# Optimization experiments

Hardware: AMD Instinct MI355X
Metric: run time of the kernel (lower is better)

Reference implementation:

```python
import jax, jax.numpy as jnp
import numpy as np

B, S, K, N = 2, 4096, 4096, 4096
BLOCKSIZE = 128  # GPTQ group size


def _unpack_rows(q):
    # int32 [K//8, N] -> int32 [K, N], 8 nibbles packed along dim 0 (little-endian)
    shifts = (jnp.arange(8, dtype=jnp.int32) * 4)
    nib = (q[:, None, :] >> shifts[None, :, None]) & 0xF  # [K//8, 8, N]
    return nib.reshape(q.shape[0] * 8, q.shape[1])


def _unpack_cols(q):
    # int32 [G, N//8] -> int32 [G, N], 8 nibbles packed along dim 1
    shifts = (jnp.arange(8, dtype=jnp.int32) * 4)
    nib = (q[:, :, None] >> shifts[None, None, :]) & 0xF  # [G, N//8, 8]
    return nib.reshape(q.shape[0], q.shape[1] * 8)


def _dequant(qweight, scales, qzeros, blocksize):
    # GPTQ int4 dequant: w[k, n] = (q[k, n] - z[g, n]) * s[g, n], g = k // blocksize
    w_int = _unpack_rows(qweight).astype(jnp.float32)          # [K, N]
    zeros = _unpack_cols(qzeros).astype(jnp.float32)           # [G, N]
    z = jnp.repeat(zeros, blocksize, axis=0)                   # [K, N]
    s = jnp.repeat(scales, blocksize, axis=0)                  # [K, N]
    return (w_int - z) * s


def setup_inputs() -> dict:
    key = jax.random.key(0)
    ks = jax.random.split(key, 6)
    inp = jax.random.normal(ks[0], (B, S, K), dtype=jnp.float32)
    residual = jax.random.normal(ks[1], (B, S, N), dtype=jnp.float32)
    qweight = jax.random.randint(ks[2], (K // 8, N), 0, 2147483647, dtype=jnp.int32)
    qzeros = jax.random.randint(ks[3], (K // BLOCKSIZE, N // 8), 0, 2147483647, dtype=jnp.int32)
    scales = jax.random.uniform(ks[4], (K // BLOCKSIZE, N), dtype=jnp.float32, minval=1e-3, maxval=1e-2)
    bias = jax.random.normal(ks[5], (N,), dtype=jnp.float32)
    return {"input": inp, "residual": residual, "qweight": qweight,
            "scales": scales, "qzeros": qzeros, "bias": bias}


def reference(input, residual, qweight, scales, qzeros, bias):
    # Fused: dequant(int4 GPTQ) -> GEMM -> +bias -> +residual (mm_bias_add_int4)
    w = _dequant(qweight, scales, qzeros, BLOCKSIZE)           # [K, N]
    out = jnp.einsum('bsk,kn->bsn', input, w) + bias + residual
    return out
```

## Files before the change

### kernel.cpp

```cpp
#include <hip/hip_runtime.h>
#include <hip/hip_bf16.h>
#include <stdint.h>

using bf16 = __hip_bfloat16;
typedef __attribute__((ext_vector_type(8))) short short8;
typedef __attribute__((ext_vector_type(4))) float floatx4;

#define DEVINL __device__ __forceinline__

constexpr int K_DIM = 4096;
constexpr int N_DIM = 4096;
constexpr int M_DIM = 8192;

constexpr int BM = 128, BN = 128, BK = 32;
constexpr int NBLK_N = N_DIM / BN;

DEVINL void gload_lds16(const void* g, void* l) {
  __builtin_amdgcn_global_load_lds((const __attribute__((address_space(1))) void*)g,
                                   (__attribute__((address_space(3))) void*)l,
                                   16, 0, 0);
}

__global__ __launch_bounds__(256) void k_a_convert(const float* __restrict__ a,
                                                   bf16* __restrict__ o) {
  int t = blockIdx.x * 256 + threadIdx.x;
  const float4* a4 = (const float4*)a;
  float4 v0 = a4[2 * t], v1 = a4[2 * t + 1];
  bf16 h[8];
  h[0] = __float2bfloat16(v0.x); h[1] = __float2bfloat16(v0.y);
  h[2] = __float2bfloat16(v0.z); h[3] = __float2bfloat16(v0.w);
  h[4] = __float2bfloat16(v1.x); h[5] = __float2bfloat16(v1.y);
  h[6] = __float2bfloat16(v1.z); h[7] = __float2bfloat16(v1.w);
  ((uint4*)o)[t] = *(const uint4*)h;
}

__global__ __launch_bounds__(256) void k_dequant(const int* __restrict__ qw,
                                                 const float* __restrict__ scales,
                                                 const int* __restrict__ qz,
                                                 bf16* __restrict__ wt) {
  __shared__ __align__(16) uint4 lds[32 * 8];
  const int b = blockIdx.x;
  const int kp0 = (b & 63) * 8;
  const int n0  = (b >> 6) * 32;
  const int t = threadIdx.x;
  const int n_l = t & 31, kp_l = t >> 5;
  const int n = n0 + n_l, kp = kp0 + kp_l;

  int q = qw[kp * N_DIM + n];
  int g = kp0 >> 4;
  float s = scales[g * N_DIM + n];
  int zword = qz[g * (N_DIM / 8) + (n >> 3)];
  float z = (float)((zword >> ((n & 7) * 4)) & 0xF);
  float nzs = -z * s;
  bf16 h[8];
#pragma unroll
  for (int i = 0; i < 8; ++i) {
    float w = fmaf((float)((q >> (4 * i)) & 0xF), s, nzs);
    h[i] = __float2bfloat16(w);
  }
  lds[n_l * 8 + (kp_l ^ (n_l & 7))] = *(const uint4*)h;
  __syncthreads();
  const int n_o = t >> 3, kp_o = t & 7;
  uint4 v = lds[n_o * 8 + (kp_o ^ (n_o & 7))];
  ((uint4*)wt)[(size_t)(n0 + n_o) * (K_DIM / 8) + kp0 + kp_o] = v;
}

template <bool A_IS_BF16>
__global__ __launch_bounds__(256, 2) void k_gemm(const void* __restrict__ a_ptr,
                                                 const bf16* __restrict__ wt,
                                                 const float* __restrict__ bias,
                                                 const float* __restrict__ residual,
                                                 float* __restrict__ out) {
  __shared__ __align__(16) bf16 As[BM * BK];
  __shared__ __align__(16) bf16 Bs[BN * BK];

  const int tid  = threadIdx.x;
  const int lane = tid & 63;
  const int wave = tid >> 6;
  const int wr = wave >> 1, wc = wave & 1;
  const int quad = lane >> 4, lq = lane & 15;
  const int sw = (lane >> 1) & 3;
  const int rd_c8 = (quad ^ sw) * 8;

  const int bid = blockIdx.x;
  const int bm = bid / NBLK_N, bn = bid % NBLK_N;
  const int m0 = bm * BM, n0 = bn * BN;

  floatx4 acc[4][4] = {};

  const int st_row = lane >> 2;
  const int st_c8  = ((lane & 3) ^ ((lane >> 3) & 3)) * 8;

  const bf16*  a_bf = (const bf16*)a_ptr;
  const float* a_f  = (const float*)a_ptr;

  for (int k0 = 0; k0 < K_DIM; k0 += BK) {
    __syncthreads();
#pragma unroll
    for (int j = 0; j < 2; ++j) {
      int q = wave + j * 4;
      const bf16* g = wt + (size_t)(n0 + q * 16 + st_row) * K_DIM + k0 + st_c8;
      gload_lds16(g, &Bs[q * 512]);
    }
    if (A_IS_BF16) {
#pragma unroll
      for (int j = 0; j < 2; ++j) {
        int q = wave + j * 4;
        const bf16* g = a_bf + (size_t)(m0 + q * 16 + st_row) * K_DIM + k0 + st_c8;
        gload_lds16(g, &As[q * 512]);
      }
    } else {
      int row = tid >> 1, c0 = (tid & 1) * 2;
      int rsw = (row >> 1) & 3;
      const float* srcf = a_f + (size_t)(m0 + row) * K_DIM + k0 + c0 * 8;
      float4 v0 = ((const float4*)srcf)[0];
      float4 v1 = ((const float4*)srcf)[1];
      float4 v2 = ((const float4*)srcf)[2];
      float4 v3 = ((const float4*)srcf)[3];
      bf16 h[16];
      h[0]  = __float2bfloat16(v0.x); h[1]  = __float2bfloat16(v0.y);
      h[2]  = __float2bfloat16(v0.z); h[3]  = __float2bfloat16(v0.w);
      h[4]  = __float2bfloat16(v1.x); h[5]  = __float2bfloat16(v1.y);
      h[6]  = __float2bfloat16(v1.z); h[7]  = __float2bfloat16(v1.w);
      h[8]  = __float2bfloat16(v2.x); h[9]  = __float2bfloat16(v2.y);
      h[10] = __float2bfloat16(v2.z); h[11] = __float2bfloat16(v2.w);
      h[12] = __float2bfloat16(v3.x); h[13] = __float2bfloat16(v3.y);
      h[14] = __float2bfloat16(v3.z); h[15] = __float2bfloat16(v3.w);
      *(uint4*)&As[row * BK + ((c0 ^ rsw) * 8)]       = *(const uint4*)h;
      *(uint4*)&As[row * BK + (((c0 + 1) ^ rsw) * 8)] = *(const uint4*)(h + 8);
    }
    __syncthreads();

    short8 afr[4], bfr[4];
#pragma unroll
    for (int mi = 0; mi < 4; ++mi)
      afr[mi] = *(const short8*)&As[(wr * 64 + mi * 16 + lq) * BK + rd_c8];
#pragma unroll
    for (int ni = 0; ni < 4; ++ni)
      bfr[ni] = *(const short8*)&Bs[(wc * 64 + ni * 16 + lq) * BK + rd_c8];
#pragma unroll
    for (int mi = 0; mi < 4; ++mi)
#pragma unroll
      for (int ni = 0; ni < 4; ++ni)
        acc[mi][ni] = __builtin_amdgcn_mfma_f32_16x16x32_bf16(afr[mi], bfr[ni],
                                                              acc[mi][ni], 0, 0, 0);
  }

#pragma unroll
  for (int ni = 0; ni < 4; ++ni) {
    int col = n0 + wc * 64 + ni * 16 + lq;
    float bv = bias[col];
#pragma unroll
    for (int mi = 0; mi < 4; ++mi) {
      int rbase = m0 + wr * 64 + mi * 16 + quad * 4;
#pragma unroll
      for (int r = 0; r < 4; ++r) {
        size_t idx = (size_t)(rbase + r) * N_DIM + col;
        out[idx] = acc[mi][ni][r] + bv + residual[idx];
      }
    }
  }
}

extern "C" void kernel_launch(void* const* d_in, const int* in_sizes, int n_in,
                              void* d_out, int out_size, void* d_ws, size_t ws_size,
                              hipStream_t stream) {
  const float* input    = (const float*)d_in[0];
  const float* residual = (const float*)d_in[1];
  const int*   qweight  = (const int*)d_in[2];
  const float* scales   = (const float*)d_in[3];
  const int*   qzeros   = (const int*)d_in[4];
  const float* bias     = (const float*)d_in[5];
  float* out = (float*)d_out;

  const size_t wt_bytes = (size_t)N_DIM * K_DIM * sizeof(bf16);
  const size_t a_bytes  = (size_t)M_DIM * K_DIM * sizeof(bf16);

  bf16* wt = (bf16*)d_ws;
  k_dequant<<<64 * 128, 256, 0, stream>>>(qweight, scales, qzeros, wt);

  if (ws_size >= wt_bytes + a_bytes) {
    bf16* a_bf = (bf16*)((char*)d_ws + wt_bytes);
    k_a_convert<<<(M_DIM * K_DIM / 8) / 256, 256, 0, stream>>>(input, a_bf);
    k_gemm<true><<<(M_DIM / BM) * (N_DIM / BN), 256, 0, stream>>>(a_bf, wt, bias, residual, out);
  } else {
    k_gemm<false><<<(M_DIM / BM) * (N_DIM / BN), 256, 0, stream>>>(input, wt, bias, residual, out);
  }
}
```

Baseline: 648.6 us.

## Double GEMM K-tile to 64 with 8-way XOR swizzle and XCD-aware block mapping

Raises the K tile from 32 to 64, so each loop iteration does two MFMA sub-steps and the number of barrier round trips halves. LDS loads and reads switch to an 8-chunk XOR swizzle to avoid bank conflicts on the wider rows. Blocks are remapped so that each XCD gets a contiguous group of 4 N-column tiles, which should improve L2 reuse of the weight tiles. The cost is more LDS per block (32KB instead of 16KB), which could limit occupancy.

```diff
diff --git a/kernel.cpp b/kernel.cpp
--- a/kernel.cpp
+++ b/kernel.cpp
@@ -12,8 +12,9 @@
 constexpr int N_DIM = 4096;
 constexpr int M_DIM = 8192;
 
-constexpr int BM = 128, BN = 128, BK = 32;
+constexpr int BM = 128, BN = 128, BK = 64;
 constexpr int NBLK_N = N_DIM / BN;
+constexpr int NBLK_M = M_DIM / BM;
 
 DEVINL void gload_lds16(const void* g, void* l) {
   __builtin_amdgcn_global_load_lds((const __attribute__((address_space(1))) void*)g,
@@ -79,17 +80,19 @@
   const int wave = tid >> 6;
   const int wr = wave >> 1, wc = wave & 1;
   const int quad = lane >> 4, lq = lane & 15;
-  const int sw = (lane >> 1) & 3;
-  const int rd_c8 = (quad ^ sw) * 8;
 
-  const int bid = blockIdx.x;
-  const int bm = bid / NBLK_N, bn = bid % NBLK_N;
+  const int xcd = blockIdx.x & 7;
+  const int idx = blockIdx.x >> 3;
+  const int bn = xcd * 4 + (idx & 3);
+  const int bm = idx >> 2;
   const int m0 = bm * BM, n0 = bn * BN;
 
   floatx4 acc[4][4] = {};
 
-  const int st_row = lane >> 2;
-  const int st_c8  = ((lane & 3) ^ ((lane >> 3) & 3)) * 8;
+  const int st_r8 = lane >> 3;
+  const int st_ce = ((lane & 7) ^ (st_r8 & 7)) * 8;
+
+  const int rd_x = lq & 7;
 
   const bf16*  a_bf = (const bf16*)a_ptr;
   const float* a_f  = (const float*)a_ptr;
@@ -97,53 +100,55 @@
   for (int k0 = 0; k0 < K_DIM; k0 += BK) {
     __syncthreads();
 #pragma unroll
-    for (int j = 0; j < 2; ++j) {
-      int q = wave + j * 4;
-      const bf16* g = wt + (size_t)(n0 + q * 16 + st_row) * K_DIM + k0 + st_c8;
-      gload_lds16(g, &Bs[q * 512]);
+    for (int j = 0; j < 4; ++j) {
+      int g = wave + j * 4;
+      const bf16* gp = wt + (size_t)(n0 + g * 8 + st_r8) * K_DIM + k0 + st_ce;
+      gload_lds16(gp, &Bs[g * 512]);
     }
     if (A_IS_BF16) {
 #pragma unroll
-      for (int j = 0; j < 2; ++j) {
-        int q = wave + j * 4;
-        const bf16* g = a_bf + (size_t)(m0 + q * 16 + st_row) * K_DIM + k0 + st_c8;
-        gload_lds16(g, &As[q * 512]);
+      for (int j = 0; j < 4; ++j) {
+        int g = wave + j * 4;
+        const bf16* gp = a_bf + (size_t)(m0 + g * 8 + st_r8) * K_DIM + k0 + st_ce;
+        gload_lds16(gp, &As[g * 512]);
       }
     } else {
-      int row = tid >> 1, c0 = (tid & 1) * 2;
-      int rsw = (row >> 1) & 3;
-      const float* srcf = a_f + (size_t)(m0 + row) * K_DIM + k0 + c0 * 8;
-      float4 v0 = ((const float4*)srcf)[0];
-      float4 v1 = ((const float4*)srcf)[1];
-      float4 v2 = ((const float4*)srcf)[2];
-      float4 v3 = ((const float4*)srcf)[3];
-      bf16 h[16];
-      h[0]  = __float2bfloat16(v0.x); h[1]  = __float2bfloat16(v0.y);
-      h[2]  = __float2bfloat16(v0.z); h[3]  = __float2bfloat16(v0.w);
-      h[4]  = __float2bfloat16(v1.x); h[5]  = __float2bfloat16(v1.y);
-      h[6]  = __float2bfloat16(v1.z); h[7]  = __float2bfloat16(v1.w);
-      h[8]  = __float2bfloat16(v2.x); h[9]  = __float2bfloat16(v2.y);
-      h[10] = __float2bfloat16(v2.z); h[11] = __float2bfloat16(v2.w);
-      h[12] = __float2bfloat16(v3.x); h[13] = __float2bfloat16(v3.y);
-      h[14] = __float2bfloat16(v3.z); h[15] = __float2bfloat16(v3.w);
-      *(uint4*)&As[row * BK + ((c0 ^ rsw) * 8)]       = *(const uint4*)h;
-      *(uint4*)&As[row * BK + (((c0 + 1) ^ rsw) * 8)] = *(const uint4*)(h + 8);
+      int row = tid >> 1, half = tid & 1;
+      int rx = row & 7;
+      const float* srcf = a_f + (size_t)(m0 + row) * K_DIM + k0 + half * 32;
+#pragma unroll
+      for (int cc = 0; cc < 4; ++cc) {
+        int logc = half * 4 + cc;
+        float4 v0 = ((const float4*)srcf)[cc * 2];
+        float4 v1 = ((const float4*)srcf)[cc * 2 + 1];
+        bf16 h[8];
+        h[0] = __float2bfloat16(v0.x); h[1] = __float2bfloat16(v0.y);
+        h[2] = __float2bfloat16(v0.z); h[3] = __float2bfloat16(v0.w);
+        h[4] = __float2bfloat16(v1.x); h[5] = __float2bfloat16(v1.y);
+        h[6] = __float2bfloat16(v1.z); h[7] = __float2bfloat16(v1.w);
+        *(uint4*)&As[row * BK + ((logc ^ rx) * 8)] = *(const uint4*)h;
+      }
     }
     __syncthreads();
 
-    short8 afr[4], bfr[4];
 #pragma unroll
-    for (int mi = 0; mi < 4; ++mi)
-      afr[mi] = *(const short8*)&As[(wr * 64 + mi * 16 + lq) * BK + rd_c8];
+    for (int s = 0; s < 2; ++s) {
+      short8 afr[4], bfr[4];
 #pragma unroll
-    for (int ni = 0; ni < 4; ++ni)
-      bfr[ni] = *(const short8*)&Bs[(wc * 64 + ni * 16 + lq) * BK + rd_c8];
-#pragma unroll
-    for (int mi = 0; mi < 4; ++mi)
+      for (int mi = 0; mi < 4; ++mi)
+        afr[mi] = *(const short8*)&As[(wr * 64 + mi * 16 + lq) * BK +
+                                      (((s * 4 + quad) ^ rd_x) * 8)];
 #pragma unroll
       for (int ni = 0; ni < 4; ++ni)
-        acc[mi][ni] = __builtin_amdgcn_mfma_f32_16x16x32_bf16(afr[mi], bfr[ni],
-                                                              acc[mi][ni], 0, 0, 0);
+        bfr[ni] = *(const short8*)&Bs[(wc * 64 + ni * 16 + lq) * BK +
+                                      (((s * 4 + quad) ^ rd_x) * 8)];
+#pragma unroll
+      for (int mi = 0; mi < 4; ++mi)
+#pragma unroll
+        for (int ni = 0; ni < 4; ++ni)
+          acc[mi][ni] = __builtin_amdgcn_mfma_f32_16x16x32_bf16(afr[mi], bfr[ni],
+                                                                acc[mi][ni], 0, 0, 0);
+    }
   }
 
 #pragma unroll
@@ -155,8 +160,8 @@
       int rbase = m0 + wr * 64 + mi * 16 + quad * 4;
 #pragma unroll
       for (int r = 0; r < 4; ++r) {
-        size_t idx = (size_t)(rbase + r) * N_DIM + col;
-        out[idx] = acc[mi][ni][r] + bv + residual[idx];
+        size_t idxo = (size_t)(rbase + r) * N_DIM + col;
+        out[idxo] = acc[mi][ni][r] + bv + residual[idxo];
       }
     }
   }
@@ -182,8 +187,8 @@
   if (ws_size >= wt_bytes + a_bytes) {
     bf16* a_bf = (bf16*)((char*)d_ws + wt_bytes);
     k_a_convert<<<(M_DIM * K_DIM / 8) / 256, 256, 0, stream>>>(input, a_bf);
-    k_gemm<true><<<(M_DIM / BM) * (N_DIM / BN), 256, 0, stream>>>(a_bf, wt, bias, residual, out);
+    k_gemm<true><<<NBLK_M * NBLK_N, 256, 0, stream>>>(a_bf, wt, bias, residual, out);
   } else {
-    k_gemm<false><<<(M_DIM / BM) * (N_DIM / BN), 256, 0, stream>>>(input, wt, bias, residual, out);
+    k_gemm<false><<<NBLK_M * NBLK_N, 256, 0, stream>>>(input, wt, bias, residual, out);
   }
 }
```

Result: faster. 594.8 us (-8.3%).
